# Optimization experiments

Measured on AMD Instinct MI355X. Metric: run time of the kernel, lower is better.

## Reference

```python
import jax, jax.numpy as jnp
import numpy as np

B, T, C, H = 8, 2048, 1024, 64  # batch, time(block_size), n_embd, head_size


def setup_inputs() -> dict:
    key = jax.random.key(0)
    k1, k2, k3, k4 = jax.random.split(key, 4)
    x = jax.random.normal(k1, (B, T, C), dtype=jnp.float32)
    # nn.Linear(n_embd, head_size, bias=False): y = x @ W.T with W [H, C];
    # store as [C, H] so projection is x @ W.
    Wq = jax.random.normal(k2, (C, H), dtype=jnp.float32) * 0.02
    Wk = jax.random.normal(k3, (C, H), dtype=jnp.float32) * 0.02
    Wv = jax.random.normal(k4, (C, H), dtype=jnp.float32) * 0.02
    return {"x": x, "Wq": Wq, "Wk": Wk, "Wv": Wv}


def reference(x, Wq, Wk, Wv):
    # x: [B, T, C]
    Bb, Tt, Cc = x.shape
    q = x @ Wq  # [B, T, H]
    k = x @ Wk  # [B, T, H]
    v = x @ Wv  # [B, T, H]
    # scores = Q @ K^T / sqrt(channels)  -- note: code scales by n_embd, not head_size
    scale = jnp.asarray(Cc, x.dtype) ** 0.5
    scores = jnp.einsum('bth,bsh->bts', q, k) / scale  # [B, T, T]
    # causal mask (decoder=True): lower-triangular allowed
    causal = jnp.tril(jnp.ones((Tt, Tt), dtype=bool))
    scores = jnp.where(causal, scores, -jnp.inf)
    attn = jax.nn.softmax(scores, axis=-1)  # [B, T, T]
    # dropout p=0.0 -> identity
    res = attn @ v  # [B, T, H]
    return res, attn
```

## Files before the change

### kernel.cpp

```cpp
#include <hip/hip_runtime.h>
#include <hip/hip_bf16.h>


typedef __attribute__((ext_vector_type(8))) short bf16x8;
typedef __attribute__((ext_vector_type(4))) float f32x4;

#define NB 8
#define NT 2048
#define NC 1024
#define NH 64

#define VM_DRAIN() asm volatile("s_waitcnt vmcnt(0)" ::: "memory")

__device__ __forceinline__ unsigned short f2bf(float f) {
    unsigned int u = __builtin_bit_cast(unsigned int, f);
    u += 0x7fffu + ((u >> 16) & 1u);
    return (unsigned short)(u >> 16);
}

__device__ __forceinline__ bf16x8 cvt8(float4 a, float4 b) {
    union { bf16x8 v; __hip_bfloat162 h[4]; } u;
    u.h[0] = __float22bfloat162_rn(make_float2(a.x, a.y));
    u.h[1] = __float22bfloat162_rn(make_float2(a.z, a.w));
    u.h[2] = __float22bfloat162_rn(make_float2(b.x, b.y));
    u.h[3] = __float22bfloat162_rn(make_float2(b.z, b.w));
    return u.v;
}

__device__ __forceinline__ void async_ld16(const void* g, const void* l) {
    __builtin_amdgcn_global_load_lds(
        (const __attribute__((address_space(1))) unsigned int*)g,
        (__attribute__((address_space(3))) unsigned int*)(unsigned int)(unsigned long long)l,
        16, 0, 0);
}

__global__ __launch_bounds__(256) void wt_kernel(
        const float* __restrict__ Wq,
        const float* __restrict__ Wk,
        const float* __restrict__ Wv,
        unsigned short* __restrict__ Wt) {
    __shared__ float tile[64][65];
    int m  = blockIdx.x >> 4;
    int k0 = (blockIdx.x & 15) * 64;
    const float* W = (m == 0) ? Wq : ((m == 1) ? Wk : Wv);
    int tid = threadIdx.x;
    for (int i = 0; i < 4; ++i) {
        int f = tid + i * 256;
        int r = f >> 4, c4 = (f & 15) * 4;
        float4 v = *(const float4*)&W[(size_t)(k0 + r) * 64 + c4];
        tile[r][c4 + 0] = v.x; tile[r][c4 + 1] = v.y;
        tile[r][c4 + 2] = v.z; tile[r][c4 + 3] = v.w;
    }
    __syncthreads();
    int n  = tid & 63;
    int kq = (tid >> 6) * 16;
    float scale = (m == 0) ? 0.03125f : 1.0f;
    __attribute__((aligned(16))) unsigned short outv[16];
    for (int j = 0; j < 16; ++j)
        outv[j] = f2bf(tile[kq + j][n] * scale);
    unsigned short* dst = &Wt[(size_t)m * (64 * 1024) + (size_t)n * 1024 + k0 + kq];
    *(uint4*)dst       = *(const uint4*)&outv[0];
    *(uint4*)(dst + 8) = *(const uint4*)&outv[8];
}

__global__ __launch_bounds__(256) void qkv_kernel(
        const float* __restrict__ x,
        const unsigned short* __restrict__ Wt,
        unsigned short* __restrict__ qkv,
        unsigned short* __restrict__ v_t) {
    __shared__ char smem[65536];

    int tid  = threadIdx.x;
    int wave = tid >> 6, lane = tid & 63, quad = lane >> 4, l15 = lane & 15;
    int row0 = blockIdx.x * 32;

    f32x4 acc[2][3];
#pragma unroll
    for (int rt = 0; rt < 2; ++rt)
#pragma unroll
        for (int j = 0; j < 3; ++j) acc[rt][j] = (f32x4){0.f, 0.f, 0.f, 0.f};

#pragma unroll
    for (int i = 0; i < 2; ++i) {
        int s = i * 256 + tid;
        int m = s >> 4, p = s & 15;
        int j = (p & 8) | ((p & 7) ^ (m & 7));
        async_ld16(x + (size_t)(row0 + m) * NC + j * 4,
                   smem + i * 4096 + wave * 1024);
    }
#pragma unroll
    for (int i = 0; i < 6; ++i) {
        int s = i * 256 + tid;
        int n = s >> 3, p = s & 7;
        int j = p ^ (n & 7);
        async_ld16(Wt + (size_t)n * NC + j * 8,
                   smem + 8192 + i * 4096 + wave * 1024);
    }

    int cur = 0;
    for (int kb = 0; kb < 16; ++kb) {
        VM_DRAIN();
        __syncthreads();
        if (kb < 15) {
            char* nb = smem + (cur ^ 1) * 32768;
#pragma unroll
            for (int i = 0; i < 2; ++i) {
                int s = i * 256 + tid;
                int m = s >> 4, p = s & 15;
                int j = (p & 8) | ((p & 7) ^ (m & 7));
                async_ld16(x + (size_t)(row0 + m) * NC + (kb + 1) * 64 + j * 4,
                           nb + i * 4096 + wave * 1024);
            }
#pragma unroll
            for (int i = 0; i < 6; ++i) {
                int s = i * 256 + tid;
                int n = s >> 3, p = s & 7;
                int j = p ^ (n & 7);
                async_ld16(Wt + (size_t)n * NC + (kb + 1) * 64 + j * 8,
                           nb + 8192 + i * 4096 + wave * 1024);
            }
        }
        char* Ab = smem + cur * 32768;
        char* Bb = Ab + 8192;
#pragma unroll
        for (int c = 0; c < 2; ++c) {
            bf16x8 af[2];
#pragma unroll
            for (int rt = 0; rt < 2; ++rt) {
                int m  = rt * 16 + l15;
                int j0 = c * 8 + quad * 2;
                int p0 = (j0 & 8) | ((j0 & 7) ^ (m & 7));
                int p1 = (j0 & 8) | (((j0 + 1) & 7) ^ (m & 7));
                float4 a0 = *(const float4*)(Ab + m * 256 + p0 * 16);
                float4 a1 = *(const float4*)(Ab + m * 256 + p1 * 16);
                af[rt] = cvt8(a0, a1);
            }
#pragma unroll
            for (int jj = 0; jj < 3; ++jj) {
                int n = (wave * 3 + jj) * 16 + l15;
                int p = (c * 4 + quad) ^ (n & 7);
                bf16x8 bf = *(const bf16x8*)(Bb + n * 128 + p * 16);
#pragma unroll
                for (int rt = 0; rt < 2; ++rt)
                    acc[rt][jj] = __builtin_amdgcn_mfma_f32_16x16x32_bf16(
                        af[rt], bf, acc[rt][jj], 0, 0, 0);
            }
        }
        cur ^= 1;
    }

    int b = row0 >> 11;
#pragma unroll
    for (int jj = 0; jj < 3; ++jj) {
        int g   = wave * 3 + jj;
        int mat = g >> 2;
        int col = (g & 3) * 16 + l15;
#pragma unroll
        for (int rt = 0; rt < 2; ++rt) {
            int rowb = row0 + rt * 16 + quad * 4;
            if (mat < 2) {
#pragma unroll
                for (int r = 0; r < 4; ++r)
                    qkv[(size_t)mat * (16384 * 64) + (size_t)(rowb + r) * 64 + col] =
                        f2bf(acc[rt][jj][r]);
            } else {
                union { unsigned long long q; unsigned short us[4]; } pk;
#pragma unroll
                for (int r = 0; r < 4; ++r) pk.us[r] = f2bf(acc[rt][jj][r]);
                *(unsigned long long*)&v_t[((size_t)b * 64 + col) * NT + (rowb & 2047)] = pk.q;
            }
        }
    }
}

__global__ __launch_bounds__(256) void lsum_kernel(
        const unsigned short* __restrict__ qg,
        const unsigned short* __restrict__ kg,
        float* __restrict__ l) {
    __shared__ unsigned short kt[2 * 64 * 64];
    char* ktb = (char*)kt;
    int tid  = threadIdx.x;
    int wave = tid >> 6, lane = tid & 63, quad = lane >> 4, l15 = lane & 15;
    int it = blockIdx.x >> 3, qq = blockIdx.x & 7;
    int b  = blockIdx.y;
    if (qq > it) return;
    int t0 = it * 64;
    size_t brow = (size_t)b * NT;

    bf16x8 qf[2];
    {
        const unsigned short* qp = qg + (brow + t0 + wave * 16 + l15) * NH + quad * 8;
        qf[0] = *(const bf16x8*)qp;
        qf[1] = *(const bf16x8*)(qp + 32);
    }
    int trow[4];
#pragma unroll
    for (int r = 0; r < 4; ++r) trow[r] = t0 + wave * 16 + quad * 4 + r;

#pragma unroll
    for (int i = 0; i < 2; ++i) {
        int s = i * 256 + tid;
        int r = s >> 3, p = s & 7;
        int j = p ^ (r & 7);
        async_ld16(kg + (brow + qq * 64 + r) * NH + j * 8,
                   ktb + i * 4096 + wave * 1024);
    }

    float rs[4] = {0.f, 0.f, 0.f, 0.f};
    int cur = 0;

    for (int st = qq; st <= it; st += 8) {
        VM_DRAIN();
        __syncthreads();
        if (st + 8 <= it) {
#pragma unroll
            for (int i = 0; i < 2; ++i) {
                int s = i * 256 + tid;
                int r = s >> 3, p = s & 7;
                int j = p ^ (r & 7);
                async_ld16(kg + (brow + (st + 8) * 64 + r) * NH + j * 8,
                           ktb + (cur ^ 1) * 8192 + i * 4096 + wave * 1024);
            }
        }
        char* kb = ktb + cur * 8192;

        f32x4 sacc[4];
#pragma unroll
        for (int nt = 0; nt < 4; ++nt) sacc[nt] = (f32x4){0.f, 0.f, 0.f, 0.f};
#pragma unroll
        for (int c = 0; c < 2; ++c)
#pragma unroll
            for (int nt = 0; nt < 4; ++nt) {
                int n = nt * 16 + l15;
                int p = (c * 4 + quad) ^ (n & 7);
                bf16x8 kf = *(const bf16x8*)(kb + n * 128 + p * 16);
                sacc[nt] = __builtin_amdgcn_mfma_f32_16x16x32_bf16(qf[c], kf, sacc[nt], 0, 0, 0);
            }
        bool dia = (st == it);
#pragma unroll
        for (int nt = 0; nt < 4; ++nt) {
            int s_g = st * 64 + nt * 16 + l15;
#pragma unroll
            for (int r = 0; r < 4; ++r) {
                float e = __expf(sacc[nt][r]);
                if (dia && s_g > trow[r]) e = 0.f;
                rs[r] += e;
            }
        }
        cur ^= 1;
    }
#pragma unroll
    for (int r = 0; r < 4; ++r) {
        float v = rs[r];
        v += __shfl_xor(v, 1, 16);
        v += __shfl_xor(v, 2, 16);
        v += __shfl_xor(v, 4, 16);
        v += __shfl_xor(v, 8, 16);
        if (l15 == 0)
            unsafeAtomicAdd(&l[brow + trow[r]], v);
    }
}

__global__ __launch_bounds__(256) void attn_m_kernel(
        const unsigned short* __restrict__ qg,
        const unsigned short* __restrict__ kg,
        const unsigned short* __restrict__ vtg,
        const float* __restrict__ l,
        float* __restrict__ res,
        float* __restrict__ attn) {
    __shared__ unsigned short kt[2 * 64 * 64];
    __shared__ unsigned short vt[2 * 64 * 64];
    __shared__ float ptf[4 * 16 * 68];
    char* ktb = (char*)kt;
    char* vtb = (char*)vt;

    int tid  = threadIdx.x;
    int wave = tid >> 6, lane = tid & 63, quad = lane >> 4, l15 = lane & 15;
    int it = blockIdx.x >> 3, qq = blockIdx.x & 7;
    int b  = blockIdx.y;
    if (qq > it) return;
    int t0 = it * 64;
    size_t brow = (size_t)b * NT;

    bf16x8 qf[2];
    {
        const unsigned short* qp = qg + (brow + t0 + wave * 16 + l15) * NH + quad * 8;
        qf[0] = *(const bf16x8*)qp;
        qf[1] = *(const bf16x8*)(qp + 32);
    }
    int trow[4];
    float rinv[4];
#pragma unroll
    for (int r = 0; r < 4; ++r) {
        trow[r] = t0 + wave * 16 + quad * 4 + r;
        rinv[r] = 1.0f / l[brow + trow[r]];
    }

    f32x4 oacc[4];
#pragma unroll
    for (int nt = 0; nt < 4; ++nt) oacc[nt] = (f32x4){0.f, 0.f, 0.f, 0.f};

#pragma unroll
    for (int i = 0; i < 2; ++i) {
        int s = i * 256 + tid;
        int r = s >> 3, p = s & 7;
        int j = p ^ (r & 7);
        async_ld16(kg + (brow + qq * 64 + r) * NH + j * 8,
                   ktb + i * 4096 + wave * 1024);
        async_ld16(vtg + ((size_t)b * 64 + r) * NT + qq * 64 + j * 8,
                   vtb + i * 4096 + wave * 1024);
    }

    int cur = 0;
    for (int st = qq; st <= it; st += 8) {
        VM_DRAIN();
        __syncthreads();
        if (st + 8 <= it) {
#pragma unroll
            for (int i = 0; i < 2; ++i) {
                int s = i * 256 + tid;
                int r = s >> 3, p = s & 7;
                int j = p ^ (r & 7);
                async_ld16(kg + (brow + (st + 8) * 64 + r) * NH + j * 8,
                           ktb + (cur ^ 1) * 8192 + i * 4096 + wave * 1024);
                async_ld16(vtg + ((size_t)b * 64 + r) * NT + (st + 8) * 64 + j * 8,
                           vtb + (cur ^ 1) * 8192 + i * 4096 + wave * 1024);
            }
        }
        char* kb = ktb + cur * 8192;
        char* vb = vtb + cur * 8192;

        f32x4 sacc[4];
#pragma unroll
        for (int nt = 0; nt < 4; ++nt) sacc[nt] = (f32x4){0.f, 0.f, 0.f, 0.f};
#pragma unroll
        for (int c = 0; c < 2; ++c)
#pragma unroll
            for (int nt = 0; nt < 4; ++nt) {
                int n = nt * 16 + l15;
                int p = (c * 4 + quad) ^ (n & 7);
                bf16x8 kf = *(const bf16x8*)(kb + n * 128 + p * 16);
                sacc[nt] = __builtin_amdgcn_mfma_f32_16x16x32_bf16(qf[c], kf, sacc[nt], 0, 0, 0);
            }

        bool dia = (st == it);
#pragma unroll
        for (int nt = 0; nt < 4; ++nt) {
            int s_g = st * 64 + nt * 16 + l15;
#pragma unroll
            for (int r = 0; r < 4; ++r) {
                float p = __expf(sacc[nt][r]) * rinv[r];
                if (dia && s_g > trow[r]) p = 0.f;
                ptf[wave * 1088 + (quad * 4 + r) * 68 + nt * 16 + l15] = p;
            }
        }
        asm volatile("s_waitcnt lgkmcnt(0)" ::: "memory");

#pragma unroll
        for (int r = 0; r < 4; ++r) {
            int row = quad * 4 + r;
            float4 pv = *(const float4*)&ptf[wave * 1088 + row * 68 + l15 * 4];
            *(float4*)&attn[(brow + t0 + wave * 16 + row) * NT + st * 64 + l15 * 4] = pv;
        }

        if (st < it) {
            float4 z4 = {0.f, 0.f, 0.f, 0.f};
#pragma unroll
            for (int k = 0; k < 4; ++k) {
                int f = tid + k * 256;
                int r = f >> 4, c4 = (f & 15) * 4;
                *(float4*)&attn[(brow + st * 64 + r) * NT + t0 + c4] = z4;
            }
        }

#pragma unroll
        for (int c = 0; c < 2; ++c) {
            const float* pp = &ptf[wave * 1088 + l15 * 68 + c * 32 + quad * 8];
            float4 a0 = *(const float4*)pp;
            float4 a1 = *(const float4*)(pp + 4);
            bf16x8 pf = cvt8(a0, a1);
#pragma unroll
            for (int nt = 0; nt < 4; ++nt) {
                int n = nt * 16 + l15;
                int p = (c * 4 + quad) ^ (n & 7);
                bf16x8 vf = *(const bf16x8*)(vb + n * 128 + p * 16);
                oacc[nt] = __builtin_amdgcn_mfma_f32_16x16x32_bf16(pf, vf, oacc[nt], 0, 0, 0);
            }
        }
        cur ^= 1;
    }

#pragma unroll
    for (int nt = 0; nt < 4; ++nt)
#pragma unroll
        for (int r = 0; r < 4; ++r)
            unsafeAtomicAdd(&res[(brow + trow[r]) * NH + nt * 16 + l15], oacc[nt][r]);
}

extern "C" void kernel_launch(void* const* d_in, const int* in_sizes, int n_in,
                              void* d_out, int out_size, void* d_ws, size_t ws_size,
                              hipStream_t stream) {
    const float* x  = (const float*)d_in[0];
    const float* Wq = (const float*)d_in[1];
    const float* Wk = (const float*)d_in[2];
    const float* Wv = (const float*)d_in[3];

    unsigned short* ws  = (unsigned short*)d_ws;
    unsigned short* Wt  = ws;
    unsigned short* qkv = ws + 3 * 64 * 1024;
    unsigned short* v_t = qkv + 2 * 16384 * 64;
    float* l = (float*)(v_t + 16384 * 64);

    float* res  = (float*)d_out;
    float* attn = res + (size_t)NB * NT * NH;

    hipMemsetAsync(l, 0, (size_t)NB * NT * sizeof(float), stream);
    hipMemsetAsync(res, 0, (size_t)NB * NT * NH * sizeof(float), stream);

    hipLaunchKernelGGL(wt_kernel, dim3(48), dim3(256), 0, stream, Wq, Wk, Wv, Wt);
    hipLaunchKernelGGL(qkv_kernel, dim3(512), dim3(256), 0, stream, x, Wt, qkv, v_t);

    const unsigned short* qg = qkv;
    const unsigned short* kg = qkv + 16384 * 64;

    hipLaunchKernelGGL(lsum_kernel, dim3(256, 8), dim3(256), 0, stream, qg, kg, l);
    hipLaunchKernelGGL(attn_m_kernel, dim3(256, 8), dim3(256), 0, stream,
                       qg, kg, v_t, l, res, attn);
}
```

Before: 227.2 us.

## Fuse row-sum and attention passes into one kernel with attn rescale pass

```diff
diff --git a/kernel.cpp b/kernel.cpp
--- a/kernel.cpp
+++ b/kernel.cpp
@@ -173,82 +173,139 @@
     }
 }
 
-__global__ __launch_bounds__(256) void lsum_kernel(
+__global__ __launch_bounds__(256) void fattn_kernel(
         const unsigned short* __restrict__ qg,
         const unsigned short* __restrict__ kg,
-        float* __restrict__ l) {
+        const unsigned short* __restrict__ vtg,
+        float* __restrict__ res,
+        float* __restrict__ attn) {
     __shared__ unsigned short kt[2 * 64 * 64];
+    __shared__ unsigned short vt[2 * 64 * 64];
+    __shared__ float ptf[32 * 68];
+    __shared__ float rsred[2][32];
+    __shared__ float rinv_s[32];
     char* ktb = (char*)kt;
-    int tid  = threadIdx.x;
+    char* vtb = (char*)vt;
+
+    int gx  = blockIdx.x;
+    int b   = blockIdx.y;
+    int rsp = gx & 1;
+    int j   = gx >> 1;
+    int it  = (b & 4) ? (31 - j) : j;
+    int tid = threadIdx.x;
     int wave = tid >> 6, lane = tid & 63, quad = lane >> 4, l15 = lane & 15;
-    int it = blockIdx.x >> 3, qq = blockIdx.x & 7;
-    int b  = blockIdx.y;
-    if (qq > it) return;
-    int t0 = it * 64;
+    int wr = wave & 1, wc = wave >> 1;
+    int tb = it * 64 + rsp * 32;
     size_t brow = (size_t)b * NT;
 
     bf16x8 qf[2];
     {
-        const unsigned short* qp = qg + (brow + t0 + wave * 16 + l15) * NH + quad * 8;
+        const unsigned short* qp = qg + (brow + tb + wr * 16 + l15) * NH + quad * 8;
         qf[0] = *(const bf16x8*)qp;
         qf[1] = *(const bf16x8*)(qp + 32);
     }
     int trow[4];
 #pragma unroll
-    for (int r = 0; r < 4; ++r) trow[r] = t0 + wave * 16 + quad * 4 + r;
+    for (int r = 0; r < 4; ++r) trow[r] = tb + wr * 16 + quad * 4 + r;
+
+    float rs[4] = {0.f, 0.f, 0.f, 0.f};
+    f32x4 oacc[2];
+    oacc[0] = (f32x4){0.f, 0.f, 0.f, 0.f};
+    oacc[1] = (f32x4){0.f, 0.f, 0.f, 0.f};
 
 #pragma unroll
     for (int i = 0; i < 2; ++i) {
         int s = i * 256 + tid;
         int r = s >> 3, p = s & 7;
-        int j = p ^ (r & 7);
-        async_ld16(kg + (brow + qq * 64 + r) * NH + j * 8,
+        int jj = p ^ (r & 7);
+        async_ld16(kg + (brow + r) * NH + jj * 8,
                    ktb + i * 4096 + wave * 1024);
-    }
-
-    float rs[4] = {0.f, 0.f, 0.f, 0.f};
+        async_ld16(vtg + ((size_t)b * 64 + r) * NT + jj * 8,
+                   vtb + i * 4096 + wave * 1024);
+    }
+
     int cur = 0;
-
-    for (int st = qq; st <= it; st += 8) {
+    for (int st = 0; st <= it; ++st) {
         VM_DRAIN();
         __syncthreads();
-        if (st + 8 <= it) {
+        if (st + 1 <= it) {
 #pragma unroll
             for (int i = 0; i < 2; ++i) {
                 int s = i * 256 + tid;
                 int r = s >> 3, p = s & 7;
-                int j = p ^ (r & 7);
-                async_ld16(kg + (brow + (st + 8) * 64 + r) * NH + j * 8,
+                int jj = p ^ (r & 7);
+                async_ld16(kg + (brow + (st + 1) * 64 + r) * NH + jj * 8,
                            ktb + (cur ^ 1) * 8192 + i * 4096 + wave * 1024);
+                async_ld16(vtg + ((size_t)b * 64 + r) * NT + (st + 1) * 64 + jj * 8,
+                           vtb + (cur ^ 1) * 8192 + i * 4096 + wave * 1024);
             }
         }
         char* kb = ktb + cur * 8192;
-
-        f32x4 sacc[4];
-#pragma unroll
-        for (int nt = 0; nt < 4; ++nt) sacc[nt] = (f32x4){0.f, 0.f, 0.f, 0.f};
+        char* vb = vtb + cur * 8192;
+
+        f32x4 sacc[2];
+        sacc[0] = (f32x4){0.f, 0.f, 0.f, 0.f};
+        sacc[1] = (f32x4){0.f, 0.f, 0.f, 0.f};
 #pragma unroll
         for (int c = 0; c < 2; ++c)
 #pragma unroll
-            for (int nt = 0; nt < 4; ++nt) {
-                int n = nt * 16 + l15;
+            for (int ntl = 0; ntl < 2; ++ntl) {
+                int n = wc * 32 + ntl * 16 + l15;
                 int p = (c * 4 + quad) ^ (n & 7);
                 bf16x8 kf = *(const bf16x8*)(kb + n * 128 + p * 16);
-                sacc[nt] = __builtin_amdgcn_mfma_f32_16x16x32_bf16(qf[c], kf, sacc[nt], 0, 0, 0);
-            }
+                sacc[ntl] = __builtin_amdgcn_mfma_f32_16x16x32_bf16(
+                    qf[c], kf, sacc[ntl], 0, 0, 0);
+            }
+
         bool dia = (st == it);
 #pragma unroll
-        for (int nt = 0; nt < 4; ++nt) {
-            int s_g = st * 64 + nt * 16 + l15;
+        for (int ntl = 0; ntl < 2; ++ntl) {
+            int s_g = st * 64 + wc * 32 + ntl * 16 + l15;
 #pragma unroll
             for (int r = 0; r < 4; ++r) {
-                float e = __expf(sacc[nt][r]);
+                float e = __expf(sacc[ntl][r]);
                 if (dia && s_g > trow[r]) e = 0.f;
                 rs[r] += e;
+                ptf[(wr * 16 + quad * 4 + r) * 68 + wc * 32 + ntl * 16 + l15] = e;
+            }
+        }
+        __syncthreads();
+
+#pragma unroll
+        for (int k = 0; k < 2; ++k) {
+            int f = k * 256 + tid;
+            int row = f >> 4, c4 = (f & 15) * 4;
+            *(float4*)&attn[(brow + tb + row) * NT + st * 64 + c4] =
+                *(const float4*)&ptf[row * 68 + c4];
+        }
+        if (st < it) {
+            float4 z4 = {0.f, 0.f, 0.f, 0.f};
+#pragma unroll
+            for (int k = 0; k < 2; ++k) {
+                int f = k * 256 + tid;
+                int row = f >> 4, c4 = (f & 15) * 4;
+                *(float4*)&attn[(brow + st * 64 + rsp * 32 + row) * NT + it * 64 + c4] = z4;
+            }
+        }
+
+#pragma unroll
+        for (int c = 0; c < 2; ++c) {
+            const float* pp = &ptf[(wr * 16 + l15) * 68 + c * 32 + quad * 8];
+            float4 a0 = *(const float4*)pp;
+            float4 a1 = *(const float4*)(pp + 4);
+            bf16x8 pf = cvt8(a0, a1);
+#pragma unroll
+            for (int ntl = 0; ntl < 2; ++ntl) {
+                int n = wc * 32 + ntl * 16 + l15;
+                int p = (c * 4 + quad) ^ (n & 7);
+                bf16x8 vf = *(const bf16x8*)(vb + n * 128 + p * 16);
+                oacc[ntl] = __builtin_amdgcn_mfma_f32_16x16x32_bf16(
+                    pf, vf, oacc[ntl], 0, 0, 0);
             }
         }
         cur ^= 1;
     }
+
 #pragma unroll
     for (int r = 0; r < 4; ++r) {
         float v = rs[r];
@@ -256,145 +313,32 @@
         v += __shfl_xor(v, 2, 16);
         v += __shfl_xor(v, 4, 16);
         v += __shfl_xor(v, 8, 16);
-        if (l15 == 0)
-            unsafeAtomicAdd(&l[brow + trow[r]], v);
-    }
-}
-
-__global__ __launch_bounds__(256) void attn_m_kernel(
-        const unsigned short* __restrict__ qg,
-        const unsigned short* __restrict__ kg,
-        const unsigned short* __restrict__ vtg,
-        const float* __restrict__ l,
-        float* __restrict__ res,
-        float* __restrict__ attn) {
-    __shared__ unsigned short kt[2 * 64 * 64];
-    __shared__ unsigned short vt[2 * 64 * 64];
-    __shared__ float ptf[4 * 16 * 68];
-    char* ktb = (char*)kt;
-    char* vtb = (char*)vt;
-
-    int tid  = threadIdx.x;
-    int wave = tid >> 6, lane = tid & 63, quad = lane >> 4, l15 = lane & 15;
-    int it = blockIdx.x >> 3, qq = blockIdx.x & 7;
-    int b  = blockIdx.y;
-    if (qq > it) return;
-    int t0 = it * 64;
-    size_t brow = (size_t)b * NT;
-
-    bf16x8 qf[2];
-    {
-        const unsigned short* qp = qg + (brow + t0 + wave * 16 + l15) * NH + quad * 8;
-        qf[0] = *(const bf16x8*)qp;
-        qf[1] = *(const bf16x8*)(qp + 32);
-    }
-    int trow[4];
-    float rinv[4];
-#pragma unroll
-    for (int r = 0; r < 4; ++r) {
-        trow[r] = t0 + wave * 16 + quad * 4 + r;
-        rinv[r] = 1.0f / l[brow + trow[r]];
-    }
-
-    f32x4 oacc[4];
-#pragma unroll
-    for (int nt = 0; nt < 4; ++nt) oacc[nt] = (f32x4){0.f, 0.f, 0.f, 0.f};
-
-#pragma unroll
-    for (int i = 0; i < 2; ++i) {
-        int s = i * 256 + tid;
-        int r = s >> 3, p = s & 7;
-        int j = p ^ (r & 7);
-        async_ld16(kg + (brow + qq * 64 + r) * NH + j * 8,
-                   ktb + i * 4096 + wave * 1024);
-        async_ld16(vtg + ((size_t)b * 64 + r) * NT + qq * 64 + j * 8,
-                   vtb + i * 4096 + wave * 1024);
-    }
-
-    int cur = 0;
-    for (int st = qq; st <= it; st += 8) {
-        VM_DRAIN();
-        __syncthreads();
-        if (st + 8 <= it) {
-#pragma unroll
-            for (int i = 0; i < 2; ++i) {
-                int s = i * 256 + tid;
-                int r = s >> 3, p = s & 7;
-                int j = p ^ (r & 7);
-                async_ld16(kg + (brow + (st + 8) * 64 + r) * NH + j * 8,
-                           ktb + (cur ^ 1) * 8192 + i * 4096 + wave * 1024);
-                async_ld16(vtg + ((size_t)b * 64 + r) * NT + (st + 8) * 64 + j * 8,
-                           vtb + (cur ^ 1) * 8192 + i * 4096 + wave * 1024);
-            }
-        }
-        char* kb = ktb + cur * 8192;
-        char* vb = vtb + cur * 8192;
-
-        f32x4 sacc[4];
-#pragma unroll
-        for (int nt = 0; nt < 4; ++nt) sacc[nt] = (f32x4){0.f, 0.f, 0.f, 0.f};
-#pragma unroll
-        for (int c = 0; c < 2; ++c)
-#pragma unroll
-            for (int nt = 0; nt < 4; ++nt) {
-                int n = nt * 16 + l15;
-                int p = (c * 4 + quad) ^ (n & 7);
-                bf16x8 kf = *(const bf16x8*)(kb + n * 128 + p * 16);
-                sacc[nt] = __builtin_amdgcn_mfma_f32_16x16x32_bf16(qf[c], kf, sacc[nt], 0, 0, 0);
-            }
-
-        bool dia = (st == it);
-#pragma unroll
-        for (int nt = 0; nt < 4; ++nt) {
-            int s_g = st * 64 + nt * 16 + l15;
-#pragma unroll
-            for (int r = 0; r < 4; ++r) {
-                float p = __expf(sacc[nt][r]) * rinv[r];
-                if (dia && s_g > trow[r]) p = 0.f;
-                ptf[wave * 1088 + (quad * 4 + r) * 68 + nt * 16 + l15] = p;
-            }
-        }
-        asm volatile("s_waitcnt lgkmcnt(0)" ::: "memory");
-
-#pragma unroll
-        for (int r = 0; r < 4; ++r) {
-            int row = quad * 4 + r;
-            float4 pv = *(const float4*)&ptf[wave * 1088 + row * 68 + l15 * 4];
-            *(float4*)&attn[(brow + t0 + wave * 16 + row) * NT + st * 64 + l15 * 4] = pv;
-        }
-
-        if (st < it) {
-            float4 z4 = {0.f, 0.f, 0.f, 0.f};
-#pragma unroll
-            for (int k = 0; k < 4; ++k) {
-                int f = tid + k * 256;
-                int r = f >> 4, c4 = (f & 15) * 4;
-                *(float4*)&attn[(brow + st * 64 + r) * NT + t0 + c4] = z4;
-            }
-        }
-
-#pragma unroll
-        for (int c = 0; c < 2; ++c) {
-            const float* pp = &ptf[wave * 1088 + l15 * 68 + c * 32 + quad * 8];
-            float4 a0 = *(const float4*)pp;
-            float4 a1 = *(const float4*)(pp + 4);
-            bf16x8 pf = cvt8(a0, a1);
-#pragma unroll
-            for (int nt = 0; nt < 4; ++nt) {
-                int n = nt * 16 + l15;
-                int p = (c * 4 + quad) ^ (n & 7);
-                bf16x8 vf = *(const bf16x8*)(vb + n * 128 + p * 16);
-                oacc[nt] = __builtin_amdgcn_mfma_f32_16x16x32_bf16(pf, vf, oacc[nt], 0, 0, 0);
-            }
-        }
-        cur ^= 1;
-    }
-
-#pragma unroll
-    for (int nt = 0; nt < 4; ++nt)
+        if (l15 == 0) rsred[wc][wr * 16 + quad * 4 + r] = v;
+    }
+    __syncthreads();
+    if (tid < 32) rinv_s[tid] = 1.0f / (rsred[0][tid] + rsred[1][tid]);
+    __syncthreads();
+
+#pragma unroll
+    for (int ntl = 0; ntl < 2; ++ntl)
 #pragma unroll
         for (int r = 0; r < 4; ++r)
-            unsafeAtomicAdd(&res[(brow + trow[r]) * NH + nt * 16 + l15], oacc[nt][r]);
+            res[(size_t)(brow + trow[r]) * NH + wc * 32 + ntl * 16 + l15] =
+                oacc[ntl][r] * rinv_s[wr * 16 + quad * 4 + r];
+
+    VM_DRAIN();
+    for (int st2 = 0; st2 <= it; ++st2) {
+#pragma unroll
+        for (int k = 0; k < 2; ++k) {
+            int f = k * 256 + tid;
+            int row = f >> 4, c4 = (f & 15) * 4;
+            float* p = &attn[(brow + tb + row) * NT + st2 * 64 + c4];
+            float4 v = *(const float4*)p;
+            float sc = rinv_s[row];
+            v.x *= sc; v.y *= sc; v.z *= sc; v.w *= sc;
+            *(float4*)p = v;
+        }
+    }
 }
 
 extern "C" void kernel_launch(void* const* d_in, const int* in_sizes, int n_in,
@@ -409,21 +353,16 @@
     unsigned short* Wt  = ws;
     unsigned short* qkv = ws + 3 * 64 * 1024;
     unsigned short* v_t = qkv + 2 * 16384 * 64;
-    float* l = (float*)(v_t + 16384 * 64);
 
     float* res  = (float*)d_out;
     float* attn = res + (size_t)NB * NT * NH;
 
-    hipMemsetAsync(l, 0, (size_t)NB * NT * sizeof(float), stream);
-    hipMemsetAsync(res, 0, (size_t)NB * NT * NH * sizeof(float), stream);
-
     hipLaunchKernelGGL(wt_kernel, dim3(48), dim3(256), 0, stream, Wq, Wk, Wv, Wt);
     hipLaunchKernelGGL(qkv_kernel, dim3(512), dim3(256), 0, stream, x, Wt, qkv, v_t);
 
     const unsigned short* qg = qkv;
     const unsigned short* kg = qkv + 16384 * 64;
 
-    hipLaunchKernelGGL(lsum_kernel, dim3(256, 8), dim3(256), 0, stream, qg, kg, l);
-    hipLaunchKernelGGL(attn_m_kernel, dim3(256, 8), dim3(256), 0, stream,
-                       qg, kg, v_t, l, res, attn);
-}
+    hipLaunchKernelGGL(fattn_kernel, dim3(64, 8), dim3(256), 0, stream,
+                       qg, kg, v_t, res, attn);
+}
```

New measurement: 235.8 us. 3.8% more time.
